# Optimization experiments

Measured on AMD Instinct MI355X. Metric: run time of the kernel, lower is better.

The kernel has to match this reference:

```python
import jax, jax.numpy as jnp
import numpy as np

# Rates 40MHz -> 60MHz => Fraction(1.5).limit_denominator(1000) = 3/2
UP, DOWN = 3, 2
MAX_RATE = max(UP, DOWN)
HALF_LEN = 10 * MAX_RATE                      # 30 (scipy.resample_poly default)
N_PRE_PAD = DOWN - (HALF_LEN % DOWN)          # 2
N_PRE_REMOVE = (HALF_LEN + N_PRE_PAD) // DOWN # 16
NUMTAPS_LS = 51
TAIL_ZEROS = 100
B, N = 8, 1048576


def _firwin_kaiser(numtaps, cutoff, beta):
    # scipy.signal.firwin(numtaps, cutoff, window=('kaiser', beta)), cutoff in Nyquist units
    m = np.arange(numtaps) - (numtaps - 1) / 2.0
    h = cutoff * np.sinc(cutoff * m)
    h *= np.kaiser(numtaps, beta)
    return h / h.sum()  # unit DC gain


def _band_int(k, f1, f2):
    # integral_{f1}^{f2} cos(pi*k*f) df, elementwise over integer array k
    k = np.asarray(k, dtype=float)
    safe = np.where(k == 0.0, 1.0, np.pi * k)
    return np.where(k == 0.0, f2 - f1, (np.sin(np.pi * k * f2) - np.sin(np.pi * k * f1)) / safe)


def _firls(numtaps, bands, desired):
    # Type-I linear-phase least-squares FIR (constant desired per band, unit weights)
    M = (numtaps - 1) // 2
    k = np.arange(M + 1)
    Q = np.zeros((M + 1, M + 1))
    rhs = np.zeros(M + 1)
    for f1, f2, d in zip(bands[0::2], bands[1::2], desired[0::2]):
        km = k[:, None] - k[None, :]
        kp = k[:, None] + k[None, :]
        Q += 0.5 * (_band_int(km, f1, f2) + _band_int(kp, f1, f2))
        rhs += d * _band_int(k, f1, f2)
    a = np.linalg.solve(Q, rhs)  # A(f) = sum_n a[n] cos(pi n f)
    half = a / 2.0
    half[0] = a[0]
    return np.concatenate([half[:0:-1], half])  # symmetric impulse response


def setup_inputs() -> dict:
    key = jax.random.key(0)
    x = jax.random.normal(key, (B, N), dtype=jnp.float32)
    # resample_poly anti-imaging filter, scaled by UP, with scipy's zero pre-padding
    h = _firwin_kaiser(2 * HALF_LEN + 1, 1.0 / MAX_RATE, 5.0) * UP
    h = np.concatenate([np.zeros(N_PRE_PAD), h])
    cutoff = DOWN / UP
    b = _firls(NUMTAPS_LS, [0.0, cutoff, cutoff + 0.1, 1.0], [1.0, 1.0, 0.0, 0.0])
    return {
        'x': x,
        'h_resample': jnp.asarray(h, jnp.float32),
        'b_fir': jnp.asarray(b, jnp.float32),
    }


def reference(x, h_resample, b_fir):
    b_sz, n = x.shape
    n_in = b_sz * n
    n_out = n_in * UP // DOWN + (1 if (n_in * UP) % DOWN else 0)
    xf = x.reshape(-1)
    Lh = h_resample.shape[0]
    # Fused polyphase resample: full convolution of UP-zero-stuffed signal
    # with h (flipped for true convolution), decimated by DOWN.
    y = jax.lax.conv_general_dilated(
        xf[None, None, :], h_resample[::-1][None, None, :],
        window_strides=(DOWN,), padding=[(Lh - 1, Lh - 1)],
        lhs_dilation=(UP,),
        dimension_numbers=('NCH', 'OIH', 'NCH'))[0, 0]
    u = y[N_PRE_REMOVE:N_PRE_REMOVE + n_out]               # == scipy.resample_poly
    up_padded = jnp.concatenate([u, jnp.zeros((TAIL_ZEROS,), x.dtype)])
    Lb = b_fir.shape[0]
    # lfilter(b, 1, .) == causal FIR: left-pad Lb-1 zeros, same-length output
    filt = jax.lax.conv_general_dilated(
        up_padded[None, None, :], b_fir[::-1][None, None, :],
        window_strides=(1,), padding=[(Lb - 1, 0)],
        dimension_numbers=('NCH', 'OIH', 'NCH'))[0, 0]
    total = n_out + TAIL_ZEROS
    per_b = total // b_sz
    return filt[:b_sz * per_b].reshape(b_sz, per_b)
```

## Files before the change

### kernel.cpp

```cpp
#include <hip/hip_runtime.h>


#define TPB 256
#define RPT 12
#define OTILE (TPB * RPT)
#define WREG 144
#define NTAPS 55
#define CPSTRIDE 56

#define SLOT(c) ((c) ^ (((c) >> 3) & 7))

__global__ __launch_bounds__(TPB) void prep_k(
    const float* __restrict__ x, const float* __restrict__ h,
    const float* __restrict__ b, float* __restrict__ cp,
    float* __restrict__ out, int n_in, int n_out, int out_size)
{
    __shared__ float h_s[63];
    __shared__ float b_s[51];
    __shared__ float x_s[64];
    __shared__ float u_s[50];

    const int tid = threadIdx.x;
    if (tid < 63) h_s[tid] = h[tid];
    if (tid < 51) b_s[tid] = b[tid];

    if (blockIdx.x == 0) {
        __syncthreads();
        for (int idx = tid; idx < 3 * CPSTRIDE; idx += TPB) {
            const int p = idx / CPSTRIDE;
            const int k = idx - p * CPSTRIDE;
            float acc = 0.0f;
            if (k < NTAPS) {
                const int j = p + 3 * k;
                for (int m = 0; m <= 50; ++m) {
                    const int hi = j - 2 * m;
                    if (hi >= 0 && hi <= 62) acc += b_s[m] * h_s[hi];
                }
            }
            cp[idx] = acc;
        }
    } else if (blockIdx.x == 1) {
        if (tid < 44) x_s[tid] = (tid < n_in) ? x[tid] : 0.0f;
        __syncthreads();
        if (tid < 50) {
            const int s  = 2 * tid + 32;
            const int p0 = s % 3;
            const int q  = s / 3;
            float u = 0.0f;
            #pragma unroll
            for (int i = 0; i <= 20; ++i) {
                const int xi = q - i;
                u += h_s[p0 + 3 * i] * ((xi >= 0) ? x_s[xi] : 0.0f);
            }
            u_s[tid] = u;
        }
        __syncthreads();
        if (tid < 50) {
            float acc = 0.0f;
            for (int t = 0; t <= tid; ++t) acc += b_s[tid - t] * u_s[t];
            out[tid] = acc;
        }
    } else {
        const int t0   = n_out - 50;
        const int qmin = (2 * t0 + 32) / 3;
        const int xb   = qmin - 20;
        if (tid < 64) {
            const int xi = xb + tid;
            x_s[tid] = (xi >= 0 && xi < n_in) ? x[xi] : 0.0f;
        }
        __syncthreads();
        if (tid < 50) {
            const int t  = t0 + tid;
            const int s  = 2 * t + 32;
            const int p0 = s % 3;
            const int q  = s / 3;
            const int base = q - xb;
            float u = 0.0f;
            #pragma unroll
            for (int i = 0; i <= 20; ++i)
                u += h_s[p0 + 3 * i] * x_s[base - i];
            u_s[tid] = u;
        }
        __syncthreads();
        const int n_tail = out_size - n_out;
        if (tid < n_tail) {
            float acc = 0.0f;
            for (int j = tid; j <= 49; ++j) acc += b_s[tid + 50 - j] * u_s[j];
            out[n_out + tid] = acc;
        }
    }
}

__device__ __forceinline__ float co(const int i, const int c0,
                                    const int c1, const int c2) {
    const int ln = i & 63;
    const int v = (i < 64)  ? __builtin_amdgcn_readlane(c0, ln)
                : (i < 128) ? __builtin_amdgcn_readlane(c1, ln)
                            : __builtin_amdgcn_readlane(c2, ln);
    return __int_as_float(v);
}

#define GRP12(g, A, B, C, D) {                                          \
    const float q2x = co(112 + 4*(g), cc0, cc1, cc2);                   \
    const float q2y = co(113 + 4*(g), cc0, cc1, cc2);                   \
    const float q2z = co(114 + 4*(g), cc0, cc1, cc2);                   \
    const float q2w = co(115 + 4*(g), cc0, cc1, cc2);                   \
    const float q1x = co( 56 + 4*(g), cc0, cc1, cc2);                   \
    const float q1y = co( 57 + 4*(g), cc0, cc1, cc2);                   \
    const float q1z = co( 58 + 4*(g), cc0, cc1, cc2);                   \
    const float q1w = co( 59 + 4*(g), cc0, cc1, cc2);                   \
    const float q0x = co(      4*(g), cc0, cc1, cc2);                   \
    const float q0y = co(  1 + 4*(g), cc0, cc1, cc2);                   \
    const float q0z = co(  2 + 4*(g), cc0, cc1, cc2);                   \
    const float q0w = co(  3 + 4*(g), cc0, cc1, cc2);                   \
                                                               \
    a0  += q2x * C.z;  a1  += q1x * C.w;  a2  += q0x * B.x;             \
    a3  += q2x * B.x;  a4  += q1x * B.y;  a5  += q0x * B.z;             \
    a6  += q2x * B.z;  a7  += q1x * B.w;  a8  += q0x * A.x;             \
    a9  += q2x * A.x;  a10 += q1x * A.y;  a11 += q0x * A.z;             \
                                                               \
    a0  += q2y * C.y;  a1  += q1y * C.z;  a2  += q0y * C.w;             \
    a3  += q2y * C.w;  a4  += q1y * B.x;  a5  += q0y * B.y;             \
    a6  += q2y * B.y;  a7  += q1y * B.z;  a8  += q0y * B.w;             \
    a9  += q2y * B.w;  a10 += q1y * A.x;  a11 += q0y * A.y;             \
                                                               \
    a0  += q2z * C.x;  a1  += q1z * C.y;  a2  += q0z * C.z;             \
    a3  += q2z * C.z;  a4  += q1z * C.w;  a5  += q0z * B.x;             \
    a6  += q2z * B.x;  a7  += q1z * B.y;  a8  += q0z * B.z;             \
    a9  += q2z * B.z;  a10 += q1z * B.w;  a11 += q0z * A.x;             \
                                                               \
    a0  += q2w * D.w;  a1  += q1w * C.x;  a2  += q0w * C.y;             \
    a3  += q2w * C.y;  a4  += q1w * C.z;  a5  += q0w * C.w;             \
    a6  += q2w * C.w;  a7  += q1w * B.x;  a8  += q0w * B.y;             \
    a9  += q2w * B.y;  a10 += q1w * B.z;  a11 += q0w * B.w; }

#define GRP12T(g, A, B, C) {                                            \
    const float q2x = co(112 + 4*(g), cc0, cc1, cc2);                   \
    const float q2y = co(113 + 4*(g), cc0, cc1, cc2);                   \
    const float q2z = co(114 + 4*(g), cc0, cc1, cc2);                   \
    const float q1x = co( 56 + 4*(g), cc0, cc1, cc2);                   \
    const float q1y = co( 57 + 4*(g), cc0, cc1, cc2);                   \
    const float q1z = co( 58 + 4*(g), cc0, cc1, cc2);                   \
    const float q0x = co(      4*(g), cc0, cc1, cc2);                   \
    const float q0y = co(  1 + 4*(g), cc0, cc1, cc2);                   \
    const float q0z = co(  2 + 4*(g), cc0, cc1, cc2);                   \
    a0  += q2x * C.z;  a1  += q1x * C.w;  a2  += q0x * B.x;             \
    a3  += q2x * B.x;  a4  += q1x * B.y;  a5  += q0x * B.z;             \
    a6  += q2x * B.z;  a7  += q1x * B.w;  a8  += q0x * A.x;             \
    a9  += q2x * A.x;  a10 += q1x * A.y;  a11 += q0x * A.z;             \
    a0  += q2y * C.y;  a1  += q1y * C.z;  a2  += q0y * C.w;             \
    a3  += q2y * C.w;  a4  += q1y * B.x;  a5  += q0y * B.y;             \
    a6  += q2y * B.y;  a7  += q1y * B.z;  a8  += q0y * B.w;             \
    a9  += q2y * B.w;  a10 += q1y * A.x;  a11 += q0y * A.y;             \
    a0  += q2z * C.x;  a1  += q1z * C.y;  a2  += q0z * C.z;             \
    a3  += q2z * C.z;  a4  += q1z * C.w;  a5  += q0z * B.x;             \
    a6  += q2z * B.x;  a7  += q1z * B.y;  a8  += q0z * B.z;             \
    a9  += q2z * B.z;  a10 += q1z * B.w;  a11 += q0z * A.x; }

#define EDGE_STAGE(NT) {                                                \
    const int fb0 = (NT) + 512 * w;                                     \
    _Pragma("unroll")                                                   \
    for (int s = 0; s < 3; ++s) {                                       \
        const int c = l + 64 * s;                                       \
        if (c > 141) break;                                             \
        const int fb = fb0 + 4 * c;                                     \
        float4 v;                                                       \
        v.x = (fb + 0 >= 0 && fb + 0 < n_in) ? x[fb + 0] : 0.0f;        \
        v.y = (fb + 1 >= 0 && fb + 1 < n_in) ? x[fb + 1] : 0.0f;        \
        v.z = (fb + 2 >= 0 && fb + 2 < n_in) ? x[fb + 2] : 0.0f;        \
        v.w = (fb + 3 >= 0 && fb + 3 < n_in) ? x[fb + 3] : 0.0f;        \
        xs4[wreg + SLOT(c)] = v;                                        \
    } }

#define XS(j) xs4[wreg + SLOT(2 * l + (j))]

#define TILE_COMPUTE(OB) {                                              \
    float a0 = 0.f, a1 = 0.f, a2 = 0.f, a3  = 0.f, a4  = 0.f, a5 = 0.f;\
    float a6 = 0.f, a7 = 0.f, a8 = 0.f, a9  = 0.f, a10 = 0.f, a11 = 0.f;\
    {                                                                   \
        float4 r0 = XS(15), r1 = XS(14), r2 = XS(13),                   \
               r3 = XS(12), r4 = XS(11), r5 = XS(10);                   \
        GRP12( 0, r0, r1, r2, r3);  r0 = XS(9);                         \
        GRP12( 1, r1, r2, r3, r4);  r1 = XS(8);                         \
        GRP12( 2, r2, r3, r4, r5);  r2 = XS(7);                         \
        GRP12( 3, r3, r4, r5, r0);  r3 = XS(6);                         \
        GRP12( 4, r4, r5, r0, r1);  r4 = XS(5);                         \
        GRP12( 5, r5, r0, r1, r2);  r5 = XS(4);                         \
        GRP12( 6, r0, r1, r2, r3);  r0 = XS(3);                         \
        GRP12( 7, r1, r2, r3, r4);  r1 = XS(2);                         \
        GRP12( 8, r2, r3, r4, r5);  r2 = XS(1);                         \
        GRP12( 9, r3, r4, r5, r0);  r3 = XS(0);                         \
        GRP12(10, r4, r5, r0, r1);                                      \
        GRP12(11, r5, r0, r1, r2);                                      \
        GRP12(12, r0, r1, r2, r3);                                      \
        GRP12T(13, r1, r2, r3);                                         \
    }                                                                   \
    const int ob_ = (OB);                                               \
    if (ob_ >= 50 && ob_ + 11 < n_out) {                                \
        float4* o4 = (float4*)(out + ob_);             \
        o4[0] = make_float4(a0, a1, a2,  a3);                           \
        o4[1] = make_float4(a4, a5, a6,  a7);                           \
        o4[2] = make_float4(a8, a9, a10, a11);                          \
    } else {                                                            \
        const float accs[RPT] = {a0,a1,a2,a3,a4,a5,a6,a7,a8,a9,a10,a11};\
        _Pragma("unroll")                                               \
        for (int d = 0; d < RPT; ++d) {                                 \
            const int o = ob_ + d;                                      \
            if (o >= 50 && o < n_out) out[o] = accs[d];                 \
        }                                                               \
    } }

__global__ __launch_bounds__(TPB) void fused_fast(
    const float* __restrict__ x, const float* __restrict__ cp,
    float* __restrict__ out, int n_in, int n_out)
{
    __shared__ float4 xs4[4 * WREG];

    const int tid = threadIdx.x;
    const int w   = tid >> 6;
    const int l   = tid & 63;
    const int bt  = blockIdx.x;
    const int o0  = bt * (2 * OTILE);
    const int ntA = 4096 * bt - 44;
    const int ntB = ntA + 2048;
    const int wreg = w * WREG;

    const int cc0 = __float_as_int(cp[l]);
    const int cc1 = __float_as_int(cp[l + 64]);
    const int cc2 = __float_as_int(cp[(l < 40) ? (128 + l) : 128]);

    const bool intA = (ntA >= 0) && (ntA + 2104 <= n_in);
    const bool intB = (ntB >= 0) && (ntB + 2104 <= n_in);

    float4 ga0, ga1, ga2, gb0, gb1, gb2;
    if (intA) {
        const float4* gw = (const float4*)(x + ntA) + 128 * w;
        ga0 = gw[l];
        ga1 = gw[l + 64];
        if (l < 14) ga2 = gw[l + 128];
    }
    if (intB) {
        const float4* gw = (const float4*)(x + ntB) + 128 * w;
        gb0 = gw[l];
        gb1 = gw[l + 64];
        if (l < 14) gb2 = gw[l + 128];
    }
    __builtin_amdgcn_sched_barrier(0);

    if (intA) {
        xs4[wreg + SLOT(l)]      = ga0;
        xs4[wreg + SLOT(l + 64)] = ga1;
        if (l < 14) xs4[wreg + SLOT(l + 128)] = ga2;
    } else {
        EDGE_STAGE(ntA);
    }
    TILE_COMPUTE(o0 + RPT * tid);

    if (intB) {
        xs4[wreg + SLOT(l)]      = gb0;
        xs4[wreg + SLOT(l + 64)] = gb1;
        if (l < 14) xs4[wreg + SLOT(l + 128)] = gb2;
    } else {
        EDGE_STAGE(ntB);
    }
    TILE_COMPUTE(o0 + OTILE + RPT * tid);
}

extern "C" void kernel_launch(void* const* d_in, const int* in_sizes, int n_in_arrs,
                              void* d_out, int out_size, void* d_ws, size_t ws_size,
                              hipStream_t stream) {
    const float* x = (const float*)d_in[0];
    const float* h = (const float*)d_in[1];
    const float* b = (const float*)d_in[2];
    float* out = (float*)d_out;
    float* cp  = (float*)d_ws;

    const int n_in  = in_sizes[0];
    const int n_out = (int)((long long)n_in * 3 / 2);

    prep_k<<<3, TPB, 0, stream>>>(x, h, b, cp, out, n_in, n_out, out_size);

    const int nblocks = (n_out + 2 * OTILE - 1) / (2 * OTILE);
    fused_fast<<<nblocks, TPB, 0, stream>>>(x, cp, out, n_in, n_out);
}
```

Measured before the change: 108.0 us.

## Fuse prep kernel into main kernel and compute combined coefficients per block

Removes the separate prep kernel launch. Each main block now computes the combined resample+FIR polyphase coefficients itself from h and b, after issuing its global x loads so the work can overlap them, instead of reading them from a workspace. Two extra blocks handle the head and tail edge outputs. This removes one launch and the dependency between the two kernels, but adds a 51-iteration coefficient loop per thread in every block.

```diff
diff --git a/kernel.cpp b/kernel.cpp
--- a/kernel.cpp
+++ b/kernel.cpp
@@ -6,90 +6,8 @@
 #define OTILE (TPB * RPT)
 #define WREG 144
 #define NTAPS 55
-#define CPSTRIDE 56
 
 #define SLOT(c) ((c) ^ (((c) >> 3) & 7))
-
-__global__ __launch_bounds__(TPB) void prep_k(
-    const float* __restrict__ x, const float* __restrict__ h,
-    const float* __restrict__ b, float* __restrict__ cp,
-    float* __restrict__ out, int n_in, int n_out, int out_size)
-{
-    __shared__ float h_s[63];
-    __shared__ float b_s[51];
-    __shared__ float x_s[64];
-    __shared__ float u_s[50];
-
-    const int tid = threadIdx.x;
-    if (tid < 63) h_s[tid] = h[tid];
-    if (tid < 51) b_s[tid] = b[tid];
-
-    if (blockIdx.x == 0) {
-        __syncthreads();
-        for (int idx = tid; idx < 3 * CPSTRIDE; idx += TPB) {
-            const int p = idx / CPSTRIDE;
-            const int k = idx - p * CPSTRIDE;
-            float acc = 0.0f;
-            if (k < NTAPS) {
-                const int j = p + 3 * k;
-                for (int m = 0; m <= 50; ++m) {
-                    const int hi = j - 2 * m;
-                    if (hi >= 0 && hi <= 62) acc += b_s[m] * h_s[hi];
-                }
-            }
-            cp[idx] = acc;
-        }
-    } else if (blockIdx.x == 1) {
-        if (tid < 44) x_s[tid] = (tid < n_in) ? x[tid] : 0.0f;
-        __syncthreads();
-        if (tid < 50) {
-            const int s  = 2 * tid + 32;
-            const int p0 = s % 3;
-            const int q  = s / 3;
-            float u = 0.0f;
-            #pragma unroll
-            for (int i = 0; i <= 20; ++i) {
-                const int xi = q - i;
-                u += h_s[p0 + 3 * i] * ((xi >= 0) ? x_s[xi] : 0.0f);
-            }
-            u_s[tid] = u;
-        }
-        __syncthreads();
-        if (tid < 50) {
-            float acc = 0.0f;
-            for (int t = 0; t <= tid; ++t) acc += b_s[tid - t] * u_s[t];
-            out[tid] = acc;
-        }
-    } else {
-        const int t0   = n_out - 50;
-        const int qmin = (2 * t0 + 32) / 3;
-        const int xb   = qmin - 20;
-        if (tid < 64) {
-            const int xi = xb + tid;
-            x_s[tid] = (xi >= 0 && xi < n_in) ? x[xi] : 0.0f;
-        }
-        __syncthreads();
-        if (tid < 50) {
-            const int t  = t0 + tid;
-            const int s  = 2 * t + 32;
-            const int p0 = s % 3;
-            const int q  = s / 3;
-            const int base = q - xb;
-            float u = 0.0f;
-            #pragma unroll
-            for (int i = 0; i <= 20; ++i)
-                u += h_s[p0 + 3 * i] * x_s[base - i];
-            u_s[tid] = u;
-        }
-        __syncthreads();
-        const int n_tail = out_size - n_out;
-        if (tid < n_tail) {
-            float acc = 0.0f;
-            for (int j = tid; j <= 49; ++j) acc += b_s[tid + 50 - j] * u_s[j];
-            out[n_out + tid] = acc;
-        }
-    }
-}
 
 __device__ __forceinline__ float co(const int i, const int c0,
                                     const int c1, const int c2) {
@@ -210,24 +128,84 @@
         }                                                               \
     } }
 
-__global__ __launch_bounds__(TPB) void fused_fast(
-    const float* __restrict__ x, const float* __restrict__ cp,
-    float* __restrict__ out, int n_in, int n_out)
+__global__ __launch_bounds__(TPB) void fused_all(
+    const float* __restrict__ x, const float* __restrict__ h,
+    const float* __restrict__ b, float* __restrict__ out,
+    int n_in, int n_out, int out_size, int nmain)
 {
     __shared__ float4 xs4[4 * WREG];
 
     const int tid = threadIdx.x;
+    const int bid = blockIdx.x;
+
+    if (bid >= nmain) {
+        float* const h_s = (float*)xs4;
+        float* const b_s = (float*)xs4 + 64;
+        float* const x_s = (float*)xs4 + 128;
+        float* const u_s = (float*)xs4 + 192;
+
+        if (tid < 63) h_s[tid] = h[tid];
+        if (tid < 51) b_s[tid] = b[tid];
+
+        if (bid == nmain) {
+            if (tid < 44) x_s[tid] = (tid < n_in) ? x[tid] : 0.0f;
+            __syncthreads();
+            if (tid < 50) {
+                const int s  = 2 * tid + 32;
+                const int p0 = s % 3;
+                const int q  = s / 3;
+                float u = 0.0f;
+                #pragma unroll
+                for (int i = 0; i <= 20; ++i) {
+                    const int xi = q - i;
+                    u += h_s[p0 + 3 * i] * ((xi >= 0) ? x_s[xi] : 0.0f);
+                }
+                u_s[tid] = u;
+            }
+            __syncthreads();
+            if (tid < 50) {
+                float acc = 0.0f;
+                for (int t = 0; t <= tid; ++t) acc += b_s[tid - t] * u_s[t];
+                out[tid] = acc;
+            }
+        } else {
+            const int t0   = n_out - 50;
+            const int qmin = (2 * t0 + 32) / 3;
+            const int xb   = qmin - 20;
+            if (tid < 64) {
+                const int xi = xb + tid;
+                x_s[tid] = (xi >= 0 && xi < n_in) ? x[xi] : 0.0f;
+            }
+            __syncthreads();
+            if (tid < 50) {
+                const int t  = t0 + tid;
+                const int s  = 2 * t + 32;
+                const int p0 = s % 3;
+                const int q  = s / 3;
+                const int base = q - xb;
+                float u = 0.0f;
+                #pragma unroll
+                for (int i = 0; i <= 20; ++i)
+                    u += h_s[p0 + 3 * i] * x_s[base - i];
+                u_s[tid] = u;
+            }
+            __syncthreads();
+            const int n_tail = out_size - n_out;
+            if (tid < n_tail) {
+                float acc = 0.0f;
+                for (int j = tid; j <= 49; ++j) acc += b_s[tid + 50 - j] * u_s[j];
+                out[n_out + tid] = acc;
+            }
+        }
+        return;
+    }
+
     const int w   = tid >> 6;
     const int l   = tid & 63;
-    const int bt  = blockIdx.x;
-    const int o0  = bt * (2 * OTILE);
-    const int ntA = 4096 * bt - 44;
+    const int wreg = w * WREG;
+    const int o0  = bid * (2 * OTILE);
+    const int ntA = 4096 * bid - 44;
     const int ntB = ntA + 2048;
-    const int wreg = w * WREG;
-
-    const int cc0 = __float_as_int(cp[l]);
-    const int cc1 = __float_as_int(cp[l + 64]);
-    const int cc2 = __float_as_int(cp[(l < 40) ? (128 + l) : 128]);
 
     const bool intA = (ntA >= 0) && (ntA + 2104 <= n_in);
     const bool intB = (ntB >= 0) && (ntB + 2104 <= n_in);
@@ -244,6 +222,31 @@
         gb0 = gw[l];
         gb1 = gw[l + 64];
         if (l < 14) gb2 = gw[l + 128];
+    }
+    __builtin_amdgcn_sched_barrier(0);
+
+    int cc0, cc1, cc2;
+    {
+        const int iA = l;
+        const int iB = 64 + l;
+        const int iC = (l < 40) ? (128 + l) : 128;
+        const int pA = iA / 56, kA = iA - pA * 56;
+        const int pB = iB / 56, kB = iB - pB * 56;
+        const int pC = iC / 56, kC = iC - pC * 56;
+        int jA = pA + 3 * kA;
+        int jB = pB + 3 * kB;
+        int jC = pC + 3 * kC;
+        float aA = 0.0f, aB = 0.0f, aC = 0.0f;
+        for (int m = 0; m <= 50; ++m) {
+            const float bm = b[m];
+            if (jA >= 0 && jA <= 62) aA += bm * h[jA];
+            if (jB >= 0 && jB <= 62) aB += bm * h[jB];
+            if (jC >= 0 && jC <= 62) aC += bm * h[jC];
+            jA -= 2; jB -= 2; jC -= 2;
+        }
+        cc0 = __float_as_int((kA < NTAPS) ? aA : 0.0f);
+        cc1 = __float_as_int((kB < NTAPS) ? aB : 0.0f);
+        cc2 = __float_as_int((kC < NTAPS) ? aC : 0.0f);
     }
     __builtin_amdgcn_sched_barrier(0);
 
@@ -273,13 +276,13 @@
     const float* h = (const float*)d_in[1];
     const float* b = (const float*)d_in[2];
     float* out = (float*)d_out;
-    float* cp  = (float*)d_ws;
+    (void)d_ws; (void)ws_size;
 
     const int n_in  = in_sizes[0];
     const int n_out = (int)((long long)n_in * 3 / 2);
 
-    prep_k<<<3, TPB, 0, stream>>>(x, h, b, cp, out, n_in, n_out, out_size);
-
-    const int nblocks = (n_out + 2 * OTILE - 1) / (2 * OTILE);
-    fused_fast<<<nblocks, TPB, 0, stream>>>(x, cp, out, n_in, n_out);
+    const int ntiles = (n_out + OTILE - 1) / OTILE;
+    const int nmain  = (ntiles + 1) / 2;
+    fused_all<<<nmain + 2, TPB, 0, stream>>>(x, h, b, out,
+                                             n_in, n_out, out_size, nmain);
 }
```

After: 130.6 us. 1.21x slower.
